# Kernel optimization log

Hardware: AMD Instinct MI355X
Metric: run time of the kernel (lower is better)

Reference implementation:

```python
import jax, jax.numpy as jnp
import numpy as np

E = 1024      # d_model
H = 16        # num heads
D = E // H    # head dim = 64
FF = 4096     # dim_feedforward
WIN = 128
EPS = 1e-5    # layer-norm eps
NEG = -1e9


def setup_inputs() -> dict:
    key = jax.random.key(0)
    ks = jax.random.split(key, 16)
    s = 0.02
    f32 = jnp.float32
    return {
        "src":       jax.random.normal(ks[0], (2, 2048, E), f32),
        "in_proj_w": jax.random.normal(ks[1], (3 * E, E), f32) * s,
        "in_proj_b": jnp.zeros((3 * E,), f32),
        "out_w":     jax.random.normal(ks[2], (E, E), f32) * s,
        "out_b":     jnp.zeros((E,), f32),
        "lin1_w":    jax.random.normal(ks[3], (FF, E), f32) * s,
        "lin1_b":    jnp.zeros((FF,), f32),
        "lin2_w":    jax.random.normal(ks[4], (E, FF), f32) * s,
        "lin2_b":    jnp.zeros((E,), f32),
        "ln1_g":     jnp.ones((E,), f32),
        "ln1_beta":  jnp.zeros((E,), f32),
        "ln2_g":     jnp.ones((E,), f32),
        "ln2_beta":  jnp.zeros((E,), f32),
    }


def _layer_norm(x, g, b):
    mu = x.mean(-1, keepdims=True)
    var = ((x - mu) ** 2).mean(-1, keepdims=True)
    return (x - mu) * jax.lax.rsqrt(var + EPS) * g + b


def reference(src, in_proj_w, in_proj_b, out_w, out_b,
              lin1_w, lin1_b, lin2_w, lin2_b,
              ln1_g, ln1_beta, ln2_g, ln2_beta):
    B, L, _ = src.shape  # batch_first=True
    x = src

    # fused QKV projection (torch Linear: y = x @ W.T + b)
    qkv = x @ in_proj_w.T + in_proj_b            # [B, L, 3E]
    q, k, v = jnp.split(qkv, 3, axis=-1)
    q = q.reshape(B, L, H, D)
    k = k.reshape(B, L, H, D)
    v = v.reshape(B, L, H, D)

    scores = jnp.einsum('blhd,bmhd->bhlm', q, k) / np.float32(np.sqrt(D))
    idx = jnp.arange(L)
    band = jnp.abs(idx[:, None] - idx[None, :]) <= WIN   # [L, L] allowed positions
    scores = jnp.where(band, scores, NEG)
    attn = jax.nn.softmax(scores, axis=-1)

    ctx = jnp.einsum('bhlm,bmhd->blhd', attn, v).reshape(B, L, E)
    attn_out = ctx @ out_w.T + out_b

    # post-norm transformer encoder layer (norm_first=False default)
    x = _layer_norm(x + attn_out, ln1_g, ln1_beta)
    ff = jax.nn.relu(x @ lin1_w.T + lin1_b) @ lin2_w.T + lin2_b
    return _layer_norm(x + ff, ln2_g, ln2_beta)
```

## Files before the change

### kernel.cpp

```cpp
#include <hip/hip_runtime.h>
#include <cstdint>
#include <cstddef>


typedef __attribute__((ext_vector_type(8))) short short8;
typedef __attribute__((ext_vector_type(4))) float f32x4;

__device__ __forceinline__ float b2f(unsigned short u) {
  union { unsigned int i; float f; } x; x.i = ((unsigned int)u) << 16; return x.f;
}
__device__ __forceinline__ unsigned short f2b(float f) {
  union { float f; unsigned int i; } x; x.f = f;
  unsigned int i = x.i;
  unsigned int r = (i + 0x7FFFu + ((i >> 16) & 1u)) >> 16;
  return (unsigned short)r;
}
__device__ __forceinline__ uint4 pack8(float4 f0, float4 f1) {
  uint4 r;
  r.x = (unsigned)f2b(f0.x) | ((unsigned)f2b(f0.y) << 16);
  r.y = (unsigned)f2b(f0.z) | ((unsigned)f2b(f0.w) << 16);
  r.z = (unsigned)f2b(f1.x) | ((unsigned)f2b(f1.y) << 16);
  r.w = (unsigned)f2b(f1.z) | ((unsigned)f2b(f1.w) << 16);
  return r;
}

__device__ __forceinline__ void gl_lds16(const unsigned short* g, unsigned short* l) {
  __builtin_amdgcn_global_load_lds(
      (const __attribute__((address_space(1))) unsigned int*)g,
      (__attribute__((address_space(3))) unsigned int*)l, 16, 0, 0);
}

__global__ __launch_bounds__(256) void conv_k(
    const float* __restrict__ in, unsigned short* __restrict__ out, int n)
{
  const int i = (blockIdx.x * 256 + threadIdx.x) * 8;
  if (i < n) {
    const float4 f0 = *(const float4*)(in + i);
    const float4 f1 = *(const float4*)(in + i + 4);
    *(uint4*)(out + i) = pack8(f0, f1);
  }
}

template<int RELU, int OUT32>
__global__ __launch_bounds__(256) void gemm128(
    const unsigned short* __restrict__ A, const unsigned short* __restrict__ Wb,
    const float* __restrict__ bias, void* __restrict__ out,
    int M, int N, int K)
{
  __shared__ unsigned short As[128 * 64];
  __shared__ unsigned short Bs[128 * 64];

  const int tid = threadIdx.x;
  const int lane = tid & 63, wid = tid >> 6;
  const int m0 = blockIdx.y * 128, n0 = blockIdx.x * 128;

  const unsigned short* gA[4];
  const unsigned short* gW[4];
  int ldsO[4];
#pragma unroll
  for (int i = 0; i < 4; ++i) {
    const int sl = wid * 256 + i * 64 + lane;
    const int r = sl >> 3, s = sl & 7, c = (s + r) & 7;
    gA[i] = A + (size_t)(m0 + r) * K + c * 8;
    gW[i] = Wb + (size_t)(n0 + r) * K + c * 8;
    ldsO[i] = (wid * 256 + i * 64) * 8;
  }

  const int cl = lane & 15;
  const int kg = lane >> 4;
  const int msub = (wid >> 1) * 64, nsub = (wid & 1) * 64;
  int aoff[4][2], boff[4][2];
#pragma unroll
  for (int t = 0; t < 4; ++t) {
    const int ar = msub + t * 16 + cl;
    const int br = nsub + t * 16 + cl;
#pragma unroll
    for (int ks = 0; ks < 2; ++ks) {
      aoff[t][ks] = ar * 64 + ((ks * 4 + kg - ar) & 7) * 8;
      boff[t][ks] = br * 64 + ((ks * 4 + kg - br) & 7) * 8;
    }
  }

  f32x4 acc[4][4];
#pragma unroll
  for (int i = 0; i < 4; ++i)
#pragma unroll
    for (int j = 0; j < 4; ++j) acc[i][j] = (f32x4){0.f, 0.f, 0.f, 0.f};

  const int steps = K >> 6;
  for (int s = 0; s < steps; ++s) {
#pragma unroll
    for (int i = 0; i < 4; ++i) { gl_lds16(gA[i], &As[ldsO[i]]); gA[i] += 64; }
#pragma unroll
    for (int i = 0; i < 4; ++i) { gl_lds16(gW[i], &Bs[ldsO[i]]); gW[i] += 64; }
    __syncthreads();

    short8 af[4][2], bf[4][2];
#pragma unroll
    for (int t = 0; t < 4; ++t)
#pragma unroll
      for (int ks = 0; ks < 2; ++ks) {
        af[t][ks] = *(const short8*)&As[aoff[t][ks]];
        bf[t][ks] = *(const short8*)&Bs[boff[t][ks]];
      }
#pragma unroll
    for (int mt = 0; mt < 4; ++mt)
#pragma unroll
      for (int nt = 0; nt < 4; ++nt)
#pragma unroll
        for (int ks = 0; ks < 2; ++ks)
          acc[mt][nt] = __builtin_amdgcn_mfma_f32_16x16x32_bf16(af[mt][ks], bf[nt][ks], acc[mt][nt], 0, 0, 0);
    __syncthreads();
  }

#pragma unroll
  for (int nt = 0; nt < 4; ++nt) {
    const int col = n0 + nsub + nt * 16 + cl;
    const float bvs = bias[col];
#pragma unroll
    for (int mt = 0; mt < 4; ++mt) {
#pragma unroll
      for (int r = 0; r < 4; ++r) {
        const int grow = m0 + msub + mt * 16 + kg * 4 + r;
        float v = acc[mt][nt][r] + bvs;
        if (RELU) v = fmaxf(v, 0.f);
        if (OUT32) ((float*)out)[(size_t)grow * N + col] = v;
        else       ((unsigned short*)out)[(size_t)grow * N + col] = f2b(v);
      }
    }
  }
}

template<int OUT32>
__global__ __launch_bounds__(256) void gemm64(
    const unsigned short* __restrict__ A, const unsigned short* __restrict__ Wb,
    const float* __restrict__ bias, void* __restrict__ out,
    int M, int N, int K)
{
  __shared__ unsigned short As[3][64 * 64];
  __shared__ unsigned short Bs[3][128 * 64];

  const int tid = threadIdx.x;
  const int lane = tid & 63, wid = tid >> 6;

  const int nwgx = gridDim.x;
  const int flat = blockIdx.y * nwgx + blockIdx.x;
  const int chunk = (nwgx * gridDim.y) >> 3;
  const int nf = (flat & 7) * chunk + (flat >> 3);
  const int m0 = (nf / nwgx) * 64, n0 = (nf % nwgx) * 128;

  const unsigned short* gA[2];
  const unsigned short* gW[4];
  int ldsA[2], ldsB[4];
#pragma unroll
  for (int i = 0; i < 2; ++i) {
    const int sl = wid * 128 + i * 64 + lane;
    const int r = sl >> 3, s = sl & 7, c = (s + r) & 7;
    gA[i] = A + (size_t)(m0 + r) * K + c * 8;
    ldsA[i] = (wid * 128 + i * 64) * 8;
  }
#pragma unroll
  for (int i = 0; i < 4; ++i) {
    const int sl = wid * 256 + i * 64 + lane;
    const int r = sl >> 3, s = sl & 7, c = (s + r) & 7;
    gW[i] = Wb + (size_t)(n0 + r) * K + c * 8;
    ldsB[i] = (wid * 256 + i * 64) * 8;
  }

  const int cl = lane & 15;
  const int kg = lane >> 4;
  int aoff[4][2], boff[2][2];
#pragma unroll
  for (int t = 0; t < 4; ++t) {
    const int ar = t * 16 + cl;
#pragma unroll
    for (int ks = 0; ks < 2; ++ks)
      aoff[t][ks] = ar * 64 + ((ks * 4 + kg - ar) & 7) * 8;
  }
#pragma unroll
  for (int t = 0; t < 2; ++t) {
    const int br = wid * 32 + t * 16 + cl;
#pragma unroll
    for (int ks = 0; ks < 2; ++ks)
      boff[t][ks] = br * 64 + ((ks * 4 + kg - br) & 7) * 8;
  }

  f32x4 acc[4][2];
#pragma unroll
  for (int i = 0; i < 4; ++i)
#pragma unroll
    for (int j = 0; j < 2; ++j) acc[i][j] = (f32x4){0.f, 0.f, 0.f, 0.f};

  const int steps = K >> 6;

  const int pre = steps < 3 ? steps : 3;
  for (int t = 0; t < pre; ++t) {
#pragma unroll
    for (int i = 0; i < 2; ++i) { gl_lds16(gA[i], &As[t][ldsA[i]]); gA[i] += 64; }
#pragma unroll
    for (int i = 0; i < 4; ++i) { gl_lds16(gW[i], &Bs[t][ldsB[i]]); gW[i] += 64; }
  }

  int cur = 0;
  for (int s = 0; s < steps; ++s) {
    const int rem = steps - 1 - s;
    if (rem >= 2)      asm volatile("s_waitcnt vmcnt(12)" ::: "memory");
    else if (rem == 1) asm volatile("s_waitcnt vmcnt(6)" ::: "memory");
    else               asm volatile("s_waitcnt vmcnt(0)" ::: "memory");
    __builtin_amdgcn_s_barrier();

    short8 af[4][2], bf[2][2];
#pragma unroll
    for (int t = 0; t < 4; ++t)
#pragma unroll
      for (int ks = 0; ks < 2; ++ks) af[t][ks] = *(const short8*)&As[cur][aoff[t][ks]];
#pragma unroll
    for (int t = 0; t < 2; ++t)
#pragma unroll
      for (int ks = 0; ks < 2; ++ks) bf[t][ks] = *(const short8*)&Bs[cur][boff[t][ks]];

    asm volatile("s_waitcnt lgkmcnt(0)" ::: "memory");
    __builtin_amdgcn_sched_barrier(0);
    __builtin_amdgcn_s_barrier();

    if (s + 3 < steps) {
#pragma unroll
      for (int i = 0; i < 2; ++i) { gl_lds16(gA[i], &As[cur][ldsA[i]]); gA[i] += 64; }
#pragma unroll
      for (int i = 0; i < 4; ++i) { gl_lds16(gW[i], &Bs[cur][ldsB[i]]); gW[i] += 64; }
    }

#pragma unroll
    for (int mt = 0; mt < 4; ++mt)
#pragma unroll
      for (int nt = 0; nt < 2; ++nt)
#pragma unroll
        for (int ks = 0; ks < 2; ++ks)
          acc[mt][nt] = __builtin_amdgcn_mfma_f32_16x16x32_bf16(af[mt][ks], bf[nt][ks], acc[mt][nt], 0, 0, 0);

    cur = (cur == 2) ? 0 : cur + 1;
  }

#pragma unroll
  for (int nt = 0; nt < 2; ++nt) {
    const int col = n0 + wid * 32 + nt * 16 + cl;
    const float bvs = bias[col];
#pragma unroll
    for (int mt = 0; mt < 4; ++mt) {
#pragma unroll
      for (int r = 0; r < 4; ++r) {
        const int grow = m0 + mt * 16 + kg * 4 + r;
        const float v = acc[mt][nt][r] + bvs;
        if (OUT32) ((float*)out)[(size_t)grow * N + col] = v;
        else       ((unsigned short*)out)[(size_t)grow * N + col] = f2b(v);
      }
    }
  }
}

__global__ __launch_bounds__(256) void attn_mfma(
    const unsigned short* __restrict__ qkv, unsigned short* __restrict__ ctx)
{
  __shared__ unsigned short Ks[64 * 72];
  __shared__ unsigned short Vt[64 * 72];
  __shared__ unsigned short Ps[64 * 72];

  const int tid = threadIdx.x;
  const int bid = blockIdx.x;
  const int qt = bid & 31, h = (bid >> 5) & 15, b = bid >> 9;
  const int q0 = qt * 64;
  const int wstart = max(0, q0 - 128);
  const int wend = min(2048, q0 + 64 + 128);
  const int ntile = (wend - wstart + 63) >> 6;
  const size_t rowb = (size_t)b * 2048;

  const int lane = tid & 63, wid = tid >> 6;
  const int cl = lane & 15;
  const int kq = (lane >> 4) * 8;
  const int rowg = lane >> 4;

  short8 aQ[2];
#pragma unroll
  for (int ks = 0; ks < 2; ++ks)
    aQ[ks] = *(const short8*)(qkv + (rowb + q0 + wid * 16 + cl) * 3072 + h * 64 + ks * 32 + kq);

  float m_i[4], l_i[4];
  f32x4 O[4];
#pragma unroll
  for (int r = 0; r < 4; ++r) { m_i[r] = -1.0e30f; l_i[r] = 0.f; }
#pragma unroll
  for (int nt = 0; nt < 4; ++nt) O[nt] = (f32x4){0.f, 0.f, 0.f, 0.f};

  for (int t = 0; t < ntile; ++t) {
    const int jbase = wstart + t * 64;
    __syncthreads();
    for (int idx = tid; idx < 512; idx += 256) {
      const int r = idx >> 3, c = idx & 7;
      const int jg = jbase + r;
      uint4 kv = {0u, 0u, 0u, 0u}, vv = {0u, 0u, 0u, 0u};
      if (jg < wend) {
        const size_t base = (rowb + jg) * 3072 + h * 64 + c * 8;
        kv = *(const uint4*)(qkv + base + 1024);
        vv = *(const uint4*)(qkv + base + 2048);
      }
      *(uint4*)&Ks[r * 72 + c * 8] = kv;
      const unsigned short* vs = (const unsigned short*)&vv;
#pragma unroll
      for (int ii = 0; ii < 8; ++ii) Vt[(c * 8 + ii) * 72 + r] = vs[ii];
    }
    __syncthreads();

    f32x4 S[4];
#pragma unroll
    for (int nt = 0; nt < 4; ++nt) S[nt] = (f32x4){0.f, 0.f, 0.f, 0.f};
#pragma unroll
    for (int nt = 0; nt < 4; ++nt)
#pragma unroll
      for (int ks = 0; ks < 2; ++ks) {
        const short8 bK = *(const short8*)&Ks[(nt * 16 + cl) * 72 + ks * 32 + kq];
        S[nt] = __builtin_amdgcn_mfma_f32_16x16x32_bf16(aQ[ks], bK, S[nt], 0, 0, 0);
      }

    float sc[4][4];
#pragma unroll
    for (int nt = 0; nt < 4; ++nt) {
      const int jg = jbase + nt * 16 + cl;
#pragma unroll
      for (int r = 0; r < 4; ++r) {
        const int i = q0 + wid * 16 + rowg * 4 + r;
        const bool v = (jg < wend) && (jg >= i - 128) && (jg <= i + 128);
        sc[nt][r] = v ? S[nt][r] * 0.125f : -1.0e30f;
      }
    }

    float alpha[4], p[4][4];
#pragma unroll
    for (int r = 0; r < 4; ++r) {
      float tm = fmaxf(fmaxf(sc[0][r], sc[1][r]), fmaxf(sc[2][r], sc[3][r]));
      tm = fmaxf(tm, __shfl_xor(tm, 1, 64));
      tm = fmaxf(tm, __shfl_xor(tm, 2, 64));
      tm = fmaxf(tm, __shfl_xor(tm, 4, 64));
      tm = fmaxf(tm, __shfl_xor(tm, 8, 64));
      const float mn = fmaxf(m_i[r], tm);
      alpha[r] = __expf(m_i[r] - mn);
      m_i[r] = mn;
      float ps = 0.f;
#pragma unroll
      for (int nt = 0; nt < 4; ++nt) { p[nt][r] = __expf(sc[nt][r] - mn); ps += p[nt][r]; }
      ps += __shfl_xor(ps, 1, 64);
      ps += __shfl_xor(ps, 2, 64);
      ps += __shfl_xor(ps, 4, 64);
      ps += __shfl_xor(ps, 8, 64);
      l_i[r] = l_i[r] * alpha[r] + ps;
    }

#pragma unroll
    for (int nt = 0; nt < 4; ++nt)
#pragma unroll
      for (int r = 0; r < 4; ++r)
        Ps[(wid * 16 + rowg * 4 + r) * 72 + nt * 16 + cl] = f2b(p[nt][r]);
    __syncthreads();

#pragma unroll
    for (int nt = 0; nt < 4; ++nt)
#pragma unroll
      for (int r = 0; r < 4; ++r) O[nt][r] *= alpha[r];
    short8 aP[2];
#pragma unroll
    for (int ks = 0; ks < 2; ++ks)
      aP[ks] = *(const short8*)&Ps[(wid * 16 + cl) * 72 + ks * 32 + kq];
#pragma unroll
    for (int nt = 0; nt < 4; ++nt)
#pragma unroll
      for (int ks = 0; ks < 2; ++ks) {
        const short8 bV = *(const short8*)&Vt[(nt * 16 + cl) * 72 + ks * 32 + kq];
        O[nt] = __builtin_amdgcn_mfma_f32_16x16x32_bf16(aP[ks], bV, O[nt], 0, 0, 0);
      }
  }

#pragma unroll
  for (int nt = 0; nt < 4; ++nt) {
    const int d = nt * 16 + cl;
#pragma unroll
    for (int r = 0; r < 4; ++r) {
      const int i = q0 + wid * 16 + rowg * 4 + r;
      ctx[(rowb + i) * 1024 + h * 64 + d] = f2b(O[nt][r] / l_i[r]);
    }
  }
}

template<int AF32, int BF32, int OF32>
__global__ __launch_bounds__(256) void ln_k(
    const void* __restrict__ a, const void* __restrict__ b,
    const float* __restrict__ g, const float* __restrict__ be,
    void* __restrict__ o)
{
  __shared__ float rbuf[8];
  const int tid = threadIdx.x;
  const size_t base = (size_t)blockIdx.x * 1024;
  const int lane = tid & 63, wid = tid >> 6;

  float xv[4], s = 0.f, sq = 0.f;
#pragma unroll
  for (int t = 0; t < 4; ++t) {
    const int c = tid + t * 256;
    const float av = AF32 ? ((const float*)a)[base + c]
                          : b2f(((const unsigned short*)a)[base + c]);
    const float bv = BF32 ? ((const float*)b)[base + c]
                          : b2f(((const unsigned short*)b)[base + c]);
    const float x = av + bv;
    xv[t] = x; s += x; sq += x * x;
  }
  for (int o2 = 1; o2 < 64; o2 <<= 1) { s += __shfl_xor(s, o2, 64); sq += __shfl_xor(sq, o2, 64); }
  if (lane == 0) { rbuf[wid] = s; rbuf[wid + 4] = sq; }
  __syncthreads();
  s  = rbuf[0] + rbuf[1] + rbuf[2] + rbuf[3];
  sq = rbuf[4] + rbuf[5] + rbuf[6] + rbuf[7];
  const float mean = s * (1.0f / 1024.f);
  const float var = sq * (1.0f / 1024.f) - mean * mean;
  const float rstd = rsqrtf(var + 1e-5f);
#pragma unroll
  for (int t = 0; t < 4; ++t) {
    const int c = tid + t * 256;
    const float y = (xv[t] - mean) * rstd * g[c] + be[c];
    if (OF32) ((float*)o)[base + c] = y;
    else      ((unsigned short*)o)[base + c] = f2b(y);
  }
}

extern "C" void kernel_launch(void* const* d_in, const int* in_sizes, int n_in,
                              void* d_out, int out_size, void* d_ws, size_t ws_size,
                              hipStream_t stream)
{
  (void)in_sizes; (void)n_in; (void)out_size; (void)ws_size;
  const float* src   = (const float*)d_in[0];
  const float* w_in  = (const float*)d_in[1];
  const float* b_in  = (const float*)d_in[2];
  const float* w_out = (const float*)d_in[3];
  const float* b_out = (const float*)d_in[4];
  const float* w1    = (const float*)d_in[5];
  const float* b1    = (const float*)d_in[6];
  const float* w2    = (const float*)d_in[7];
  const float* b2    = (const float*)d_in[8];
  const float* g1    = (const float*)d_in[9];
  const float* be1   = (const float*)d_in[10];
  const float* g2    = (const float*)d_in[11];
  const float* be2   = (const float*)d_in[12];

  char* ws = (char*)d_ws;
  unsigned short* srcb  = (unsigned short*)(ws);
  unsigned short* x1b   = srcb;
  unsigned short* qkv   = (unsigned short*)(ws + 8388608);
  unsigned short* ctx   = (unsigned short*)(ws + 33554432);
  unsigned short* attnb = (unsigned short*)(ws + 8388608);
  unsigned short* ff1   = (unsigned short*)(ws + 8388608);
  unsigned short* wslot = (unsigned short*)(ws + 41943040);
  float*          outf  = (float*)d_out;

  conv_k<<<dim3(2048), 256, 0, stream>>>(src, srcb, 4194304);
  conv_k<<<dim3(1536), 256, 0, stream>>>(w_in, wslot, 3145728);
  gemm128<0, 0><<<dim3(24, 32), 256, 0, stream>>>(srcb, wslot, b_in, qkv, 4096, 3072, 1024);
  attn_mfma<<<dim3(1024), 256, 0, stream>>>(qkv, ctx);
  conv_k<<<dim3(512), 256, 0, stream>>>(w_out, wslot, 1048576);
  gemm64<0><<<dim3(8, 64), 256, 0, stream>>>(ctx, wslot, b_out, attnb, 4096, 1024, 1024);
  ln_k<0, 0, 0><<<dim3(4096), 256, 0, stream>>>(srcb, attnb, g1, be1, x1b);
  conv_k<<<dim3(2048), 256, 0, stream>>>(w1, wslot, 4194304);
  gemm128<1, 0><<<dim3(32, 32), 256, 0, stream>>>(x1b, wslot, b1, ff1, 4096, 4096, 1024);
  conv_k<<<dim3(2048), 256, 0, stream>>>(w2, wslot, 4194304);
  gemm64<1><<<dim3(8, 64), 256, 0, stream>>>(ff1, wslot, b2, outf, 4096, 1024, 4096);
  ln_k<0, 1, 1><<<dim3(4096), 256, 0, stream>>>(x1b, outf, g2, be2, outf);
}
```

Measured before the change: 316.5 us.

## Double-buffer gemm128 with async prefetch, split MFMA phases, and XCD-aware block remap

Converts the 128x128 GEMM from a single-buffered load-sync-compute loop to a two-stage LDS ring. Global-to-LDS loads for step s+2 are issued while MFMAs for the current step run, and vmcnt waits replace the full syncthreads. Both GEMM kernels now split each K-step's MFMAs into two halves around the barrier, raising priority with s_setprio during the MFMA runs. The block index is also remapped so consecutive flat IDs spread across the 8 XCDs for better L2 locality. The cost is double the LDS per block, which may cut occupancy. The remap assumes the grid size is a multiple of 8.

```diff
diff --git a/kernel.cpp b/kernel.cpp
--- a/kernel.cpp
+++ b/kernel.cpp
@@ -47,12 +47,17 @@
     const float* __restrict__ bias, void* __restrict__ out,
     int M, int N, int K)
 {
-  __shared__ unsigned short As[128 * 64];
-  __shared__ unsigned short Bs[128 * 64];
+  __shared__ unsigned short As[2][128 * 64];
+  __shared__ unsigned short Bs[2][128 * 64];
 
   const int tid = threadIdx.x;
   const int lane = tid & 63, wid = tid >> 6;
-  const int m0 = blockIdx.y * 128, n0 = blockIdx.x * 128;
+
+  const int nwgx = gridDim.x;
+  const int flat = blockIdx.y * nwgx + blockIdx.x;
+  const int chunk = (nwgx * gridDim.y) >> 3;
+  const int nf = (flat & 7) * chunk + (flat >> 3);
+  const int m0 = (nf / nwgx) * 128, n0 = (nf % nwgx) * 128;
 
   const unsigned short* gA[4];
   const unsigned short* gW[4];
@@ -88,29 +93,61 @@
     for (int j = 0; j < 4; ++j) acc[i][j] = (f32x4){0.f, 0.f, 0.f, 0.f};
 
   const int steps = K >> 6;
+
+  const int pre = steps < 2 ? steps : 2;
+  for (int t = 0; t < pre; ++t) {
+#pragma unroll
+    for (int i = 0; i < 4; ++i) { gl_lds16(gA[i], &As[t][ldsO[i]]); gA[i] += 64; }
+#pragma unroll
+    for (int i = 0; i < 4; ++i) { gl_lds16(gW[i], &Bs[t][ldsO[i]]); gW[i] += 64; }
+  }
+
+  int cur = 0;
   for (int s = 0; s < steps; ++s) {
-#pragma unroll
-    for (int i = 0; i < 4; ++i) { gl_lds16(gA[i], &As[ldsO[i]]); gA[i] += 64; }
-#pragma unroll
-    for (int i = 0; i < 4; ++i) { gl_lds16(gW[i], &Bs[ldsO[i]]); gW[i] += 64; }
-    __syncthreads();
+    if (s + 1 < steps) asm volatile("s_waitcnt vmcnt(8)" ::: "memory");
+    else               asm volatile("s_waitcnt vmcnt(0)" ::: "memory");
+    __builtin_amdgcn_s_barrier();
 
     short8 af[4][2], bf[4][2];
 #pragma unroll
-    for (int t = 0; t < 4; ++t)
-#pragma unroll
-      for (int ks = 0; ks < 2; ++ks) {
-        af[t][ks] = *(const short8*)&As[aoff[t][ks]];
-        bf[t][ks] = *(const short8*)&Bs[boff[t][ks]];
-      }
+    for (int t = 0; t < 4; ++t) {
+      af[t][0] = *(const short8*)&As[cur][aoff[t][0]];
+      bf[t][0] = *(const short8*)&Bs[cur][boff[t][0]];
+    }
+#pragma unroll
+    for (int t = 0; t < 4; ++t) {
+      af[t][1] = *(const short8*)&As[cur][aoff[t][1]];
+      bf[t][1] = *(const short8*)&Bs[cur][boff[t][1]];
+    }
+
+    __builtin_amdgcn_s_setprio(1);
 #pragma unroll
     for (int mt = 0; mt < 4; ++mt)
 #pragma unroll
       for (int nt = 0; nt < 4; ++nt)
-#pragma unroll
-        for (int ks = 0; ks < 2; ++ks)
-          acc[mt][nt] = __builtin_amdgcn_mfma_f32_16x16x32_bf16(af[mt][ks], bf[nt][ks], acc[mt][nt], 0, 0, 0);
-    __syncthreads();
+        acc[mt][nt] = __builtin_amdgcn_mfma_f32_16x16x32_bf16(af[mt][0], bf[nt][0], acc[mt][nt], 0, 0, 0);
+    __builtin_amdgcn_s_setprio(0);
+
+    asm volatile("s_waitcnt lgkmcnt(0)" ::: "memory");
+    __builtin_amdgcn_sched_barrier(0);
+    __builtin_amdgcn_s_barrier();
+
+    if (s + 2 < steps) {
+#pragma unroll
+      for (int i = 0; i < 4; ++i) { gl_lds16(gA[i], &As[cur][ldsO[i]]); gA[i] += 64; }
+#pragma unroll
+      for (int i = 0; i < 4; ++i) { gl_lds16(gW[i], &Bs[cur][ldsO[i]]); gW[i] += 64; }
+    }
+
+    __builtin_amdgcn_s_setprio(1);
+#pragma unroll
+    for (int mt = 0; mt < 4; ++mt)
+#pragma unroll
+      for (int nt = 0; nt < 4; ++nt)
+        acc[mt][nt] = __builtin_amdgcn_mfma_f32_16x16x32_bf16(af[mt][1], bf[nt][1], acc[mt][nt], 0, 0, 0);
+    __builtin_amdgcn_s_setprio(0);
+
+    cur ^= 1;
   }
 
 #pragma unroll
@@ -211,13 +248,21 @@
 
     short8 af[4][2], bf[2][2];
 #pragma unroll
-    for (int t = 0; t < 4; ++t)
-#pragma unroll
-      for (int ks = 0; ks < 2; ++ks) af[t][ks] = *(const short8*)&As[cur][aoff[t][ks]];
-#pragma unroll
-    for (int t = 0; t < 2; ++t)
-#pragma unroll
-      for (int ks = 0; ks < 2; ++ks) bf[t][ks] = *(const short8*)&Bs[cur][boff[t][ks]];
+    for (int t = 0; t < 4; ++t) af[t][0] = *(const short8*)&As[cur][aoff[t][0]];
+#pragma unroll
+    for (int t = 0; t < 2; ++t) bf[t][0] = *(const short8*)&Bs[cur][boff[t][0]];
+#pragma unroll
+    for (int t = 0; t < 4; ++t) af[t][1] = *(const short8*)&As[cur][aoff[t][1]];
+#pragma unroll
+    for (int t = 0; t < 2; ++t) bf[t][1] = *(const short8*)&Bs[cur][boff[t][1]];
+
+    __builtin_amdgcn_s_setprio(1);
+#pragma unroll
+    for (int mt = 0; mt < 4; ++mt)
+#pragma unroll
+      for (int nt = 0; nt < 2; ++nt)
+        acc[mt][nt] = __builtin_amdgcn_mfma_f32_16x16x32_bf16(af[mt][0], bf[nt][0], acc[mt][nt], 0, 0, 0);
+    __builtin_amdgcn_s_setprio(0);
 
     asm volatile("s_waitcnt lgkmcnt(0)" ::: "memory");
     __builtin_amdgcn_sched_barrier(0);
@@ -230,13 +275,13 @@
       for (int i = 0; i < 4; ++i) { gl_lds16(gW[i], &Bs[cur][ldsB[i]]); gW[i] += 64; }
     }
 
+    __builtin_amdgcn_s_setprio(1);
 #pragma unroll
     for (int mt = 0; mt < 4; ++mt)
 #pragma unroll
       for (int nt = 0; nt < 2; ++nt)
-#pragma unroll
-        for (int ks = 0; ks < 2; ++ks)
-          acc[mt][nt] = __builtin_amdgcn_mfma_f32_16x16x32_bf16(af[mt][ks], bf[nt][ks], acc[mt][nt], 0, 0, 0);
+        acc[mt][nt] = __builtin_amdgcn_mfma_f32_16x16x32_bf16(af[mt][1], bf[nt][1], acc[mt][nt], 0, 0, 0);
+    __builtin_amdgcn_s_setprio(0);
 
     cur = (cur == 2) ? 0 : cur + 1;
   }
```

Result: no change. 315.3 us (-0.4%).
